# Performance work log

Hardware: AMD Instinct MI355X
Metric: run time of the kernel (lower is better)

The kernel has to match this reference:

```python
import jax, jax.numpy as jnp
import numpy as np

HEADS = 8
DIM_HEAD = 64
CHUNK = 128
EPS = 1e-6
KERNEL_EPS = 1e-4


def softmax_kernel(x, proj, is_query):
    # x: [b,h,n,d], proj: [f,d]  (FAVOR+ positive softmax features)
    d = x.shape[-1]
    data_normalizer = d ** -0.25
    ratio = proj.shape[0] ** -0.5
    data_dash = jnp.einsum('bhnd,fd->bhnf', x * data_normalizer, proj)
    diag = 0.5 * (data_normalizer ** 2) * jnp.sum(x * x, axis=-1, keepdims=True)  # [b,h,n,1]
    if is_query:
        m = jnp.max(data_dash, axis=-1, keepdims=True)
    else:
        m = jnp.max(data_dash, axis=(-1, -2), keepdims=True)
    return ratio * (jnp.exp(data_dash - diag - jax.lax.stop_gradient(m)) + KERNEL_EPS)


def infer_hidden_states(q, k, v, chunk_size=CHUNK):
    # q,k: [b,h,n,f], v: [b,h,n,e]; chunked causal linear attention with carried cumsums
    b, h, n, f = q.shape
    e = v.shape[-1]
    nc = n // chunk_size

    def to_chunks(t):
        return jnp.moveaxis(t.reshape(b, h, nc, chunk_size, t.shape[-1]), 2, 0)

    qs, ks, vs = to_chunks(q), to_chunks(k), to_chunks(v)

    def step(carry, inp):
        Z, S = carry  # [b,h,1,f], [b,h,1,f,e]
        qc, kc, vc = inp
        k_cum = Z + jnp.cumsum(kc, axis=2)                       # [b,h,c,f]
        D_inv = 1.0 / jnp.einsum('bhnf,bhnf->bhn', qc, k_cum + EPS)
        ctx = jnp.einsum('bhnf,bhne->bhnfe', kc, vc)             # [b,h,c,f,e]
        ctx_cum = S + jnp.cumsum(ctx, axis=2)
        out = jnp.einsum('bhnfe,bhnf,bhn->bhne', ctx_cum, qc, D_inv)
        return (k_cum[:, :, -1:], ctx_cum[:, :, -1:]), out

    init = (jnp.zeros((b, h, 1, f), q.dtype), jnp.zeros((b, h, 1, f, e), q.dtype))
    (Z, S), outs = jax.lax.scan(step, init, (qs, ks, vs))
    out = jnp.moveaxis(outs, 0, 2).reshape(b, h, n, e)
    return out, Z[:, :, 0], S[:, :, 0]


def reference(x, proj, Wq, Wk, Wv, Wo, bo):
    b, n, dim = x.shape
    h, dh = HEADS, DIM_HEAD

    def split_heads(t):
        return jnp.transpose(t.reshape(b, n, h, dh), (0, 2, 1, 3))

    q = split_heads(x @ Wq)
    k = split_heads(x @ Wk)
    v = split_heads(x @ Wv)

    qf = softmax_kernel(q, proj, is_query=True)
    kf = softmax_kernel(k, proj, is_query=False)

    out, Z, S = infer_hidden_states(qf, kf, v)
    out = jnp.transpose(out, (0, 2, 1, 3)).reshape(b, n, h * dh)
    out = out @ Wo + bo
    return out, Z, S


def setup_inputs() -> dict:
    key = jax.random.key(0)
    ks = jax.random.split(key, 6)
    b, n, dim = 2, 2048, 512
    f = 256
    return {
        'x': jax.random.normal(ks[0], (b, n, dim), jnp.float32),
        'proj': jax.random.normal(ks[1], (f, DIM_HEAD), jnp.float32),
        'Wq': jax.random.normal(ks[2], (dim, dim), jnp.float32) * (dim ** -0.5),
        'Wk': jax.random.normal(ks[3], (dim, dim), jnp.float32) * (dim ** -0.5),
        'Wv': jax.random.normal(ks[4], (dim, dim), jnp.float32) * (dim ** -0.5),
        'Wo': jax.random.normal(ks[5], (dim, dim), jnp.float32) * (dim ** -0.5),
        'bo': jnp.zeros((dim,), jnp.float32),
    }
```

## Files before the change

### kernel.cpp

```cpp
#include <hip/hip_runtime.h>
#include <hip/hip_bf16.h>
#include <math.h>

#define NB    2
#define NSEQ  2048
#define DIMM  512
#define NH    8
#define DHd   64
#define FF    256
#define CHK   128
#define NCHK  16
#define NBH   16

typedef unsigned short ushort_t;
typedef __attribute__((ext_vector_type(8))) __bf16 bf16x8;
typedef __attribute__((ext_vector_type(4))) float floatx4;

__device__ __forceinline__ unsigned short f2bf(float x) {
    union { __hip_bfloat16 h; unsigned short u; } v;
    v.h = __float2bfloat16(x);
    return v.u;
}
__device__ __forceinline__ float bf2f(unsigned short u) {
    union { unsigned short u2[2]; float f; } v;
    v.u2[0] = 0; v.u2[1] = u;
    return v.f;
}
__device__ __forceinline__ unsigned enc_f(float x) {
    unsigned u = __float_as_uint(x);
    return (u & 0x80000000u) ? ~u : (u | 0x80000000u);
}
__device__ __forceinline__ float dec_f(unsigned e) {
    unsigned u = (e & 0x80000000u) ? (e & 0x7fffffffu) : ~e;
    return __uint_as_float(u);
}

__device__ __forceinline__ void gload16(const void* g, void* l) {
    __builtin_amdgcn_global_load_lds(
        (const __attribute__((address_space(1))) void*)g,
        (__attribute__((address_space(3))) void*)l, 16, 0, 0);
}

__device__ __forceinline__ bf16x8 frag8(const ushort_t* lds, int row, int kb) {
    return *((const bf16x8*)lds + row * 8 + (kb ^ (row & 7)));
}
__device__ __forceinline__ bf16x8 fragS(const ushort_t* lds, int row, int kb) {
    return *((const bf16x8*)lds + row * 16 + (kb ^ (row & 15)));
}

__global__ __launch_bounds__(256)
void prep(const float* __restrict__ x, const float* __restrict__ proj,
          const float* __restrict__ W0, const float* __restrict__ W1,
          const float* __restrict__ W2, const float* __restrict__ W3,
          ushort_t* __restrict__ xb, ushort_t* __restrict__ projb,
          ushort_t* __restrict__ T0, ushort_t* __restrict__ T1,
          ushort_t* __restrict__ T2, ushort_t* __restrict__ T3,
          unsigned* __restrict__ mk_u)
{
    __shared__ float t[32][33];
    const int b = blockIdx.x, tid = threadIdx.x;
    if (b < 2048) {
        const int gid = b * 256 + tid;
        const float4 v = *(const float4*)(x + (size_t)gid * 4);
        union { ushort4 v4; unsigned short s[4]; } pk;
        pk.s[0] = f2bf(v.x); pk.s[1] = f2bf(v.y); pk.s[2] = f2bf(v.z); pk.s[3] = f2bf(v.w);
        ((ushort4*)xb)[gid] = pk.v4;
    } else if (b < 2064) {
        const int gid = (b - 2048) * 256 + tid;
        const float dn = 0.35355339059327379f;
        const float4 v = *(const float4*)(proj + (size_t)gid * 4);
        union { ushort4 v4; unsigned short s[4]; } pk;
        pk.s[0] = f2bf(v.x * dn); pk.s[1] = f2bf(v.y * dn);
        pk.s[2] = f2bf(v.z * dn); pk.s[3] = f2bf(v.w * dn);
        ((ushort4*)projb)[gid] = pk.v4;
    } else if (b < 3088) {
        const int idx = b - 2064;
        const int z = idx >> 8, rem = idx & 255;
        const int bx = rem & 15, by = rem >> 4;
        const float* W = (z == 0) ? W0 : (z == 1) ? W1 : (z == 2) ? W2 : W3;
        ushort_t* T = (z == 0) ? T0 : (z == 1) ? T1 : (z == 2) ? T2 : T3;
        const int x0 = bx * 32, y0 = by * 32;
        const int tx = tid & 31, ty = tid >> 5;
#pragma unroll
        for (int i = 0; i < 4; i++)
            t[ty + i * 8][tx] = W[(size_t)(y0 + ty + i * 8) * DIMM + x0 + tx];
        __syncthreads();
#pragma unroll
        for (int i = 0; i < 4; i++)
            T[(size_t)(x0 + ty + i * 8) * DIMM + y0 + tx] = f2bf(t[tx][ty + i * 8]);
    } else {
        if (tid < NBH) mk_u[tid] = 0u;
    }
}

__device__ __forceinline__ void mfma_mainloop(
    const ushort_t* __restrict__ AG, const ushort_t* __restrict__ BG,
    ushort_t* As, ushort_t* Bs, int ldA, int ldB, int K,
    floatx4 acc[4][4], int tid)
{
    const int lane = tid & 63, wid = tid >> 6;
    const int q = lane >> 4, c = lane & 15;
    const int wm = (wid >> 1) * 64, wn = (wid & 1) * 64;

    for (int k0 = 0; k0 < K; k0 += 64) {
#pragma unroll
        for (int t = 0; t < 4; t++) {
            const int g = t * 256 + tid, r = g >> 3, kb = (g & 7) ^ (r & 7);
            gload16(AG + (size_t)r * ldA + k0 + kb * 8, As + (size_t)g * 8);
        }
#pragma unroll
        for (int t = 0; t < 4; t++) {
            const int g = t * 256 + tid, r = g >> 3, kb = (g & 7) ^ (r & 7);
            gload16(BG + (size_t)r * ldB + k0 + kb * 8, Bs + (size_t)g * 8);
        }
        __syncthreads();
#pragma unroll
        for (int ks = 0; ks < 2; ks++) {
            bf16x8 af[4], bfr[4];
#pragma unroll
            for (int i = 0; i < 4; i++) {
                af[i]  = frag8(As, wm + i * 16 + c, ks * 4 + q);
                bfr[i] = frag8(Bs, wn + i * 16 + c, ks * 4 + q);
            }
#pragma unroll
            for (int i = 0; i < 4; i++)
#pragma unroll
                for (int j = 0; j < 4; j++)
                    acc[i][j] = __builtin_amdgcn_mfma_f32_16x16x32_bf16(
                        af[i], bfr[j], acc[i][j], 0, 0, 0);
        }
        __syncthreads();
    }
}

__global__ __launch_bounds__(256)
void gemm_qkv(const ushort_t* __restrict__ xb,
              const ushort_t* __restrict__ Wtq, const ushort_t* __restrict__ Wtk,
              const ushort_t* __restrict__ Wtv,
              ushort_t* __restrict__ qb, ushort_t* __restrict__ kb,
              ushort_t* __restrict__ vTb)
{
    __shared__ alignas(16) ushort_t SM[16896];
    ushort_t* As = SM;
    ushort_t* Bs = SM + 8192;
    const int tid = threadIdx.x;
    const int n0 = blockIdx.x * 128, m0 = blockIdx.y * 128, z = blockIdx.z;
    const ushort_t* Bt = (z == 0) ? Wtq : ((z == 1) ? Wtk : Wtv);

    floatx4 zero = {0.f, 0.f, 0.f, 0.f};
    floatx4 acc[4][4];
#pragma unroll
    for (int i = 0; i < 4; i++)
#pragma unroll
        for (int j = 0; j < 4; j++) acc[i][j] = zero;

    mfma_mainloop(xb + (size_t)m0 * DIMM, Bt + (size_t)n0 * DIMM, As, Bs,
                  DIMM, DIMM, DIMM, acc, tid);

    const int lane = tid & 63, wid = tid >> 6;
    const int q = lane >> 4, c = lane & 15;
    const int wm = (wid >> 1) * 64, wn = (wid & 1) * 64;

#pragma unroll
    for (int i = 0; i < 4; i++)
#pragma unroll
        for (int j = 0; j < 4; j++) {
            const int col = wn + j * 16 + c;
#pragma unroll
            for (int r = 0; r < 4; r++) {
                const int row = wm + i * 16 + q * 4 + r;
                SM[row * 132 + col] = f2bf(acc[i][j][r]);
            }
        }
    __syncthreads();

    if (z < 2) {
        ushort_t* ob = (z == 0) ? qb : kb;
#pragma unroll
        for (int p = 0; p < 16; p++) {
            const int idx = p * 256 + tid;
            const int row = idx >> 5, c4 = idx & 31;
            ushort4 o = *(const ushort4*)&SM[row * 132 + c4 * 4];
            *(ushort4*)(ob + (size_t)(m0 + row) * DIMM + n0 + c4 * 4) = o;
        }
    } else {
        const int bb = m0 >> 11, nbase = m0 & 2047;
#pragma unroll
        for (int p = 0; p < 16; p++) {
            const int idx = p * 256 + tid;
            const int cl2 = idx >> 5, n4 = idx & 31;
            const int C = n0 + cl2;
            const int h = C >> 6, e = C & 63;
            union { ushort4 v4; unsigned short s[4]; } pk;
#pragma unroll
            for (int k = 0; k < 4; k++) pk.s[k] = SM[(n4 * 4 + k) * 132 + cl2];
            *(ushort4*)(vTb + (((size_t)(bb * NH + h) * 64 + e)) * NSEQ + nbase + n4 * 4) = pk.v4;
        }
    }
}

__global__ __launch_bounds__(256)
void gemm_out(const ushort_t* __restrict__ attnb, const ushort_t* __restrict__ Wto,
              float* __restrict__ out, const float* __restrict__ bias)
{
    __shared__ alignas(16) ushort_t As[8192];
    __shared__ alignas(16) ushort_t Bs[8192];
    const int tid = threadIdx.x;
    const int n0 = blockIdx.x * 128, m0 = blockIdx.y * 128;

    floatx4 zero = {0.f, 0.f, 0.f, 0.f};
    floatx4 acc[4][4];
#pragma unroll
    for (int i = 0; i < 4; i++)
#pragma unroll
        for (int j = 0; j < 4; j++) acc[i][j] = zero;

    mfma_mainloop(attnb + (size_t)m0 * DIMM, Wto + (size_t)n0 * DIMM, As, Bs,
                  DIMM, DIMM, DIMM, acc, tid);

    const int lane = tid & 63, wid = tid >> 6;
    const int q = lane >> 4, c = lane & 15;
    const int wm = (wid >> 1) * 64, wn = (wid & 1) * 64;
#pragma unroll
    for (int i = 0; i < 4; i++)
#pragma unroll
        for (int j = 0; j < 4; j++) {
            const int col = n0 + wn + j * 16 + c;
            const float bv = bias[col];
#pragma unroll
            for (int r = 0; r < 4; r++) {
                const int row = m0 + wm + i * 16 + q * 4 + r;
                out[(size_t)row * DIMM + col] = acc[i][j][r] + bv;
            }
        }
}

__global__ __launch_bounds__(256)
void kmax(const ushort_t* __restrict__ kb_, const ushort_t* __restrict__ projb,
          unsigned* __restrict__ mk_u)
{
    __shared__ alignas(16) ushort_t As[8192];
    __shared__ alignas(16) ushort_t Bs[16384];
    __shared__ float red[256];
    const int tid = threadIdx.x, lane = tid & 63, wid = tid >> 6;
    const int q = lane >> 4, cl = lane & 15;
    const int m0 = blockIdx.x * 128, h = blockIdx.y;
    const int bb = m0 >> 11;
    const ushort_t* Aq = kb_ + (size_t)m0 * DIMM + h * 64;

#pragma unroll
    for (int t = 0; t < 4; t++) {
        const int g = t * 256 + tid, r = g >> 3, kb = (g & 7) ^ (r & 7);
        gload16(Aq + (size_t)r * DIMM + kb * 8, As + (size_t)g * 8);
    }
#pragma unroll
    for (int t = 0; t < 8; t++) {
        const int g = t * 256 + tid, r = g >> 3, kb = (g & 7) ^ (r & 7);
        gload16(projb + (size_t)r * 64 + kb * 8, Bs + (size_t)g * 8);
    }
    __syncthreads();

    floatx4 zero = {0.f, 0.f, 0.f, 0.f};
    floatx4 acc[4][8];
#pragma unroll
    for (int i = 0; i < 4; i++)
#pragma unroll
        for (int j = 0; j < 8; j++) acc[i][j] = zero;
    const int wm = (wid >> 1) * 64, wn = (wid & 1) * 128;
#pragma unroll
    for (int ks = 0; ks < 2; ks++) {
        bf16x8 af[4], bfr[8];
#pragma unroll
        for (int i = 0; i < 4; i++) af[i] = frag8(As, wm + i * 16 + cl, ks * 4 + q);
#pragma unroll
        for (int j = 0; j < 8; j++) bfr[j] = frag8(Bs, wn + j * 16 + cl, ks * 4 + q);
#pragma unroll
        for (int i = 0; i < 4; i++)
#pragma unroll
            for (int j = 0; j < 8; j++)
                acc[i][j] = __builtin_amdgcn_mfma_f32_16x16x32_bf16(
                    af[i], bfr[j], acc[i][j], 0, 0, 0);
    }
    float mloc = -3.0e38f;
#pragma unroll
    for (int i = 0; i < 4; i++)
#pragma unroll
        for (int j = 0; j < 8; j++)
#pragma unroll
            for (int r = 0; r < 4; r++) mloc = fmaxf(mloc, acc[i][j][r]);
    red[tid] = mloc;
    __syncthreads();
    for (int s = 128; s > 0; s >>= 1) {
        if (tid < s) red[tid] = fmaxf(red[tid], red[tid + s]);
        __syncthreads();
    }
    if (tid == 0) atomicMax(&mk_u[bb * NH + h], enc_f(red[0]));
}

__global__ __launch_bounds__(256)
void featx(const ushort_t* __restrict__ qb_, const ushort_t* __restrict__ kb_,
           const ushort_t* __restrict__ projb, const unsigned* __restrict__ mk_u,
           ushort_t* __restrict__ qfb, ushort_t* __restrict__ kfb,
           ushort_t* __restrict__ kfTb, float* __restrict__ Ksum)
{
    __shared__ alignas(16) ushort_t SM[24576];
    __shared__ float dtmp[256];
    __shared__ float diag_l[128];
    __shared__ float mx2[2][128];
    __shared__ float colp[2][256];
    ushort_t* As = SM;
    ushort_t* Bs = SM + 8192;
    const int tid = threadIdx.x, lane = tid & 63, wid = tid >> 6;
    const int q = lane >> 4, cl = lane & 15;
    const int m0 = blockIdx.x * 128, h = blockIdx.y, src = blockIdx.z;
    const int bb = m0 >> 11, nloc = m0 & 2047;
    const int bh = bb * NH + h;
    const int cidx = nloc >> 7;
    const ushort_t* Aq = (src ? kb_ : qb_) + (size_t)m0 * DIMM + h * 64;

    {
        const int row = tid >> 1, half = tid & 1;
        float s = 0.f;
        const ushort_t* p = Aq + (size_t)row * DIMM + half * 32;
#pragma unroll
        for (int d = 0; d < 32; d += 4) {
            ushort4 w = *(const ushort4*)(p + d);
            float a = bf2f(w.x), b2 = bf2f(w.y), c2 = bf2f(w.z), d2 = bf2f(w.w);
            s += a * a + b2 * b2 + c2 * c2 + d2 * d2;
        }
        dtmp[tid] = s;
    }
    __syncthreads();
    if (tid < 128) diag_l[tid] = (dtmp[2 * tid] + dtmp[2 * tid + 1]) * 0.0625f;

#pragma unroll
    for (int t = 0; t < 4; t++) {
        const int g = t * 256 + tid, r = g >> 3, kb = (g & 7) ^ (r & 7);
        gload16(Aq + (size_t)r * DIMM + kb * 8, As + (size_t)g * 8);
    }
#pragma unroll
    for (int t = 0; t < 8; t++) {
        const int g = t * 256 + tid, r = g >> 3, kb = (g & 7) ^ (r & 7);
        gload16(projb + (size_t)r * 64 + kb * 8, Bs + (size_t)g * 8);
    }
    __syncthreads();

    floatx4 zero = {0.f, 0.f, 0.f, 0.f};
    floatx4 acc[4][8];
#pragma unroll
    for (int i = 0; i < 4; i++)
#pragma unroll
        for (int j = 0; j < 8; j++) acc[i][j] = zero;
    const int wm = (wid >> 1) * 64, wn = (wid & 1) * 128;
#pragma unroll
    for (int ks = 0; ks < 2; ks++) {
        bf16x8 af[4], bfr[8];
#pragma unroll
        for (int i = 0; i < 4; i++) af[i] = frag8(As, wm + i * 16 + cl, ks * 4 + q);
#pragma unroll
        for (int j = 0; j < 8; j++) bfr[j] = frag8(Bs, wn + j * 16 + cl, ks * 4 + q);
#pragma unroll
        for (int i = 0; i < 4; i++)
#pragma unroll
            for (int j = 0; j < 8; j++)
                acc[i][j] = __builtin_amdgcn_mfma_f32_16x16x32_bf16(
                    af[i], bfr[j], acc[i][j], 0, 0, 0);
    }

    const float mk = src ? dec_f(mk_u[bh]) : 0.f;
    if (src == 0) {
#pragma unroll
        for (int i = 0; i < 4; i++)
#pragma unroll
            for (int r = 0; r < 4; r++) {
                const int row = wm + i * 16 + q * 4 + r;
                float mx = -3.0e38f;
#pragma unroll
                for (int j = 0; j < 8; j++) mx = fmaxf(mx, acc[i][j][r]);
                mx = fmaxf(mx, __shfl_xor(mx, 1)); mx = fmaxf(mx, __shfl_xor(mx, 2));
                mx = fmaxf(mx, __shfl_xor(mx, 4)); mx = fmaxf(mx, __shfl_xor(mx, 8));
                if (cl == 0) mx2[wid & 1][row] = mx;
            }
    }
    __syncthreads();

#pragma unroll
    for (int i = 0; i < 4; i++)
#pragma unroll
        for (int r = 0; r < 4; r++) {
            const int row = wm + i * 16 + q * 4 + r;
            const float cc = diag_l[row] + (src ? mk : fmaxf(mx2[0][row], mx2[1][row]));
#pragma unroll
            for (int j = 0; j < 8; j++)
                acc[i][j][r] = 0.0625f * (__expf(acc[i][j][r] - cc) + 1.0e-4f);
        }

    if (src) {
#pragma unroll
        for (int j = 0; j < 8; j++) {
            float s = 0.f;
#pragma unroll
            for (int i = 0; i < 4; i++)
                s += acc[i][j][0] + acc[i][j][1] + acc[i][j][2] + acc[i][j][3];
            s += __shfl_xor(s, 16);
            s += __shfl_xor(s, 32);
            if (q == 0) colp[wid >> 1][wn + j * 16 + cl] = s;
        }
    }

    ushort_t* ff = src ? kfb : qfb;
    const size_t frow = (size_t)bh * NSEQ + nloc;

#pragma unroll
    for (int hf = 0; hf < 2; hf++) {
        __syncthreads();
        if ((wid & 1) == hf) {
#pragma unroll
            for (int i = 0; i < 4; i++)
#pragma unroll
                for (int j = 0; j < 8; j++) {
                    const int col = j * 16 + cl;
#pragma unroll
                    for (int r = 0; r < 4; r++) {
                        const int row = wm + i * 16 + q * 4 + r;
                        SM[row * 132 + col] = f2bf(acc[i][j][r]);
                    }
                }
        }
        if (hf == 0 && src) {
            Ksum[((size_t)bh * NCHK + cidx) * FF + tid] = colp[0][tid] + colp[1][tid];
        }
        __syncthreads();
#pragma unroll
        for (int p = 0; p < 16; p++) {
            const int idx = p * 256 + tid;
            const int row = idx >> 5, c4 = idx & 31;
            ushort4 o = *(const ushort4*)&SM[row * 132 + c4 * 4];
            *(ushort4*)(ff + (frow + row) * FF + hf * 128 + c4 * 4) = o;
        }
        if (src) {
#pragma unroll
            for (int p = 0; p < 16; p++) {
                const int idx = p * 256 + tid;
                const int f = idx >> 5, n4 = idx & 31;
                union { ushort4 v4; unsigned short s[4]; } pk;
#pragma unroll
                for (int k = 0; k < 4; k++) pk.s[k] = SM[(n4 * 4 + k) * 132 + f];
                *(ushort4*)(kfTb + ((size_t)bh * FF + hf * 128 + f) * NSEQ + nloc + n4 * 4) = pk.v4;
            }
        }
    }
}

__global__ __launch_bounds__(256)
void ctx_mfma(const ushort_t* __restrict__ vTb, const ushort_t* __restrict__ kfTb,
              float* __restrict__ CTXT)
{
    __shared__ alignas(16) ushort_t As[4096];
    __shared__ alignas(16) ushort_t Bs[16384];
    const int tid = threadIdx.x, lane = tid & 63, wid = tid >> 6;
    const int q = lane >> 4, cl = lane & 15;
    const int bh = blockIdx.x >> 4, c = blockIdx.x & 15;
    const ushort_t* A = vTb + ((size_t)bh * 64) * NSEQ + c * CHK;
    const ushort_t* B = kfTb + ((size_t)bh * FF) * NSEQ + c * CHK;
    const int fw = wid * 64;

    floatx4 zero = {0.f, 0.f, 0.f, 0.f};
    floatx4 acc[4][4];
#pragma unroll
    for (int i = 0; i < 4; i++)
#pragma unroll
        for (int j = 0; j < 4; j++) acc[i][j] = zero;

    for (int k0 = 0; k0 < CHK; k0 += 64) {
#pragma unroll
        for (int t = 0; t < 2; t++) {
            const int g = t * 256 + tid, r = g >> 3, kb = (g & 7) ^ (r & 7);
            gload16(A + (size_t)r * NSEQ + k0 + kb * 8, As + (size_t)g * 8);
        }
#pragma unroll
        for (int t = 0; t < 8; t++) {
            const int g = t * 256 + tid, r = g >> 3, kb = (g & 7) ^ (r & 7);
            gload16(B + (size_t)r * NSEQ + k0 + kb * 8, Bs + (size_t)g * 8);
        }
        __syncthreads();
#pragma unroll
        for (int ks = 0; ks < 2; ks++) {
            bf16x8 af[4], bfr[4];
#pragma unroll
            for (int i = 0; i < 4; i++) {
                af[i]  = frag8(As, i * 16 + cl, ks * 4 + q);
                bfr[i] = frag8(Bs, fw + i * 16 + cl, ks * 4 + q);
            }
#pragma unroll
            for (int i = 0; i < 4; i++)
#pragma unroll
                for (int j = 0; j < 4; j++)
                    acc[i][j] = __builtin_amdgcn_mfma_f32_16x16x32_bf16(
                        af[i], bfr[j], acc[i][j], 0, 0, 0);
        }
        __syncthreads();
    }
#pragma unroll
    for (int i = 0; i < 4; i++)
#pragma unroll
        for (int j = 0; j < 4; j++) {
            const int f = fw + j * 16 + cl;
#pragma unroll
            for (int r = 0; r < 4; r++) {
                const int e = i * 16 + q * 4 + r;
                CTXT[(((size_t)bh * NCHK + c) * 64 + e) * FF + f] = acc[i][j][r];
            }
        }
}

__global__ void prefix_zs(float* __restrict__ Ksum, float* __restrict__ Zout,
                          const float* __restrict__ CTXT, ushort_t* __restrict__ ctxp,
                          float* __restrict__ Sout)
{
    const int b = blockIdx.x;
    if (b < 1024) {
        const int idx = b * 256 + threadIdx.x;
        const int bh = idx >> 14, ef = idx & 16383;
        const int e = ef >> 8, f = ef & 255;
        float run = 0.f;
#pragma unroll
        for (int c = 0; c < NCHK; c++) {
            const size_t o = (((size_t)bh * NCHK + c) * 64 + e) * FF + f;
            const float t = CTXT[o];
            ctxp[o] = f2bf(run);
            run += t;
        }
        Sout[((size_t)bh * FF + f) * 64 + e] = run;
    } else {
        const int idx = (b - 1024) * 256 + threadIdx.x;
        const int bh = idx >> 8, f = idx & 255;
        float run = 0.f;
#pragma unroll
        for (int c = 0; c < NCHK; c++) {
            const size_t o = ((size_t)(bh * NCHK + c)) * FF + f;
            const float t = Ksum[o];
            Ksum[o] = run;
            run += t;
        }
        Zout[(size_t)bh * FF + f] = run;
    }
}

__global__ __launch_bounds__(256)
void chunk_out_mfma(const ushort_t* __restrict__ qfb, const ushort_t* __restrict__ kfb,
                    const ushort_t* __restrict__ vTb, const float* __restrict__ Zex,
                    const ushort_t* __restrict__ ctxp, ushort_t* __restrict__ attnb)
{
    __shared__ alignas(16) ushort_t Sld[16384];
    __shared__ alignas(16) ushort_t As[8192];
    __shared__ alignas(16) ushort_t Bs[8192];
    __shared__ float zeps[256];
    __shared__ float rows_part[2][128];
    __shared__ float denp[256];
    __shared__ float den_l[128];

    const int tid = threadIdx.x, lane = tid & 63, wid = tid >> 6;
    const int q = lane >> 4, cl = lane & 15;
    const int bh = blockIdx.x >> 4, c = blockIdx.x & 15;
    const int bb = bh >> 3, h = bh & 7;
    const int n0 = c * CHK;
    const ushort_t* Q  = qfb + ((size_t)bh * NSEQ + n0) * FF;
    const ushort_t* Kf = kfb + ((size_t)bh * NSEQ + n0) * FF;

    zeps[tid] = Zex[((size_t)bh * NCHK + c) * FF + tid] + 1.0e-6f;

    floatx4 zero = {0.f, 0.f, 0.f, 0.f};
    floatx4 acc1[4][4];
#pragma unroll
    for (int i = 0; i < 4; i++)
#pragma unroll
        for (int j = 0; j < 4; j++) acc1[i][j] = zero;
    const int wm = (wid >> 1) * 64, wn = (wid & 1) * 64;
    for (int k0 = 0; k0 < FF; k0 += 64) {
#pragma unroll
        for (int t = 0; t < 4; t++) {
            const int g = t * 256 + tid, r = g >> 3, kb = (g & 7) ^ (r & 7);
            gload16(Q + (size_t)r * FF + k0 + kb * 8, As + (size_t)g * 8);
        }
#pragma unroll
        for (int t = 0; t < 4; t++) {
            const int g = t * 256 + tid, r = g >> 3, kb = (g & 7) ^ (r & 7);
            gload16(Kf + (size_t)r * FF + k0 + kb * 8, Bs + (size_t)g * 8);
        }
        __syncthreads();
#pragma unroll
        for (int ks = 0; ks < 2; ks++) {
            bf16x8 af[4], bfr[4];
#pragma unroll
            for (int i = 0; i < 4; i++) {
                af[i]  = frag8(As, wm + i * 16 + cl, ks * 4 + q);
                bfr[i] = frag8(Bs, wn + i * 16 + cl, ks * 4 + q);
            }
#pragma unroll
            for (int i = 0; i < 4; i++)
#pragma unroll
                for (int j = 0; j < 4; j++)
                    acc1[i][j] = __builtin_amdgcn_mfma_f32_16x16x32_bf16(
                        af[i], bfr[j], acc1[i][j], 0, 0, 0);
        }
        __syncthreads();
    }
#pragma unroll
    for (int i = 0; i < 4; i++)
#pragma unroll
        for (int r = 0; r < 4; r++) {
            const int row = wm + i * 16 + q * 4 + r;
            float part = 0.f;
#pragma unroll
            for (int j = 0; j < 4; j++) {
                const int col = wn + j * 16 + cl;
                const float v = (col <= row) ? acc1[i][j][r] : 0.f;
                part += v;
                Sld[(row * 16 + ((col >> 3) ^ (row & 15))) * 8 + (col & 7)] = f2bf(v);
            }
            part += __shfl_xor(part, 1); part += __shfl_xor(part, 2);
            part += __shfl_xor(part, 4); part += __shfl_xor(part, 8);
            if (cl == 0) rows_part[wid & 1][row] = part;
        }
    __syncthreads();

    floatx4 acc2[4][2];
#pragma unroll
    for (int i = 0; i < 4; i++)
#pragma unroll
        for (int j = 0; j < 2; j++) acc2[i][j] = zero;
    const ushort_t* Vt = vTb + ((size_t)bh * 64) * NSEQ + n0;
    for (int k0 = 0; k0 < CHK; k0 += 64) {
#pragma unroll
        for (int t = 0; t < 2; t++) {
            const int g = t * 256 + tid, r = g >> 3, kb = (g & 7) ^ (r & 7);
            gload16(Vt + (size_t)r * NSEQ + k0 + kb * 8, As + (size_t)g * 8);
        }
        __syncthreads();
#pragma unroll
        for (int ks = 0; ks < 2; ks++) {
            bf16x8 af[4], bfr[2];
            const int kbS = (k0 >> 3) + ks * 4 + q;
#pragma unroll
            for (int i = 0; i < 4; i++) af[i] = frag8(As, i * 16 + cl, ks * 4 + q);
#pragma unroll
            for (int j = 0; j < 2; j++) bfr[j] = fragS(Sld, wid * 32 + j * 16 + cl, kbS);
#pragma unroll
            for (int i = 0; i < 4; i++)
#pragma unroll
                for (int j = 0; j < 2; j++)
                    acc2[i][j] = __builtin_amdgcn_mfma_f32_16x16x32_bf16(
                        af[i], bfr[j], acc2[i][j], 0, 0, 0);
        }
        __syncthreads();
    }

    const ushort_t* Cp = ctxp + ((size_t)bh * NCHK + c) * 64 * FF;
    float dacc = 0.f;
    const int drow = tid & 127, dhalf = tid >> 7;
    for (int k0 = 0; k0 < FF; k0 += 64) {
#pragma unroll
        for (int t = 0; t < 2; t++) {
            const int g = t * 256 + tid, r = g >> 3, kb = (g & 7) ^ (r & 7);
            gload16(Cp + (size_t)r * FF + k0 + kb * 8, As + (size_t)g * 8);
        }
#pragma unroll
        for (int t = 0; t < 4; t++) {
            const int g = t * 256 + tid, r = g >> 3, kb = (g & 7) ^ (r & 7);
            gload16(Q + (size_t)r * FF + k0 + kb * 8, Bs + (size_t)g * 8);
        }
        __syncthreads();
#pragma unroll
        for (int ks = 0; ks < 2; ks++) {
            bf16x8 af[4], bfr[2];
#pragma unroll
            for (int i = 0; i < 4; i++) af[i] = frag8(As, i * 16 + cl, ks * 4 + q);
#pragma unroll
            for (int j = 0; j < 2; j++) bfr[j] = frag8(Bs, wid * 32 + j * 16 + cl, ks * 4 + q);
#pragma unroll
            for (int i = 0; i < 4; i++)
#pragma unroll
                for (int j = 0; j < 2; j++)
                    acc2[i][j] = __builtin_amdgcn_mfma_f32_16x16x32_bf16(
                        af[i], bfr[j], acc2[i][j], 0, 0, 0);
        }
#pragma unroll
        for (int gi = 0; gi < 4; gi++) {
            const int kb = dhalf * 4 + gi;
            const ushort_t* gp = Bs + ((size_t)drow * 8 + (kb ^ (drow & 7))) * 8;
            const int kbase = k0 + kb * 8;
#pragma unroll
            for (int e2 = 0; e2 < 8; e2++)
                dacc = fmaf(bf2f(gp[e2]), zeps[kbase + e2], dacc);
        }
        __syncthreads();
    }
    denp[tid] = dacc;
    __syncthreads();
    if (tid < 128)
        den_l[tid] = rows_part[0][tid] + rows_part[1][tid] + denp[tid] + denp[tid + 128];
    __syncthreads();

#pragma unroll
    for (int j = 0; j < 2; j++) {
        const int row = wid * 32 + j * 16 + cl;
        const float dinv = 1.0f / den_l[row];
#pragma unroll
        for (int i = 0; i < 4; i++)
#pragma unroll
            for (int r = 0; r < 4; r++) {
                const int e = i * 16 + q * 4 + r;
                Sld[row * 68 + e] = f2bf(acc2[i][j][r] * dinv);
            }
    }
    __syncthreads();
#pragma unroll
    for (int p = 0; p < 8; p++) {
        const int idx = p * 256 + tid;
        const int row = idx >> 4, e4 = idx & 15;
        ushort4 o = *(const ushort4*)&Sld[row * 68 + e4 * 4];
        *(ushort4*)(attnb + ((size_t)(bb * NSEQ + n0 + row)) * DIMM + h * 64 + e4 * 4) = o;
    }
}

extern "C" void kernel_launch(void* const* d_in, const int* in_sizes, int n_in,
                              void* d_out, int out_size, void* d_ws, size_t ws_size,
                              hipStream_t stream)
{
    (void)in_sizes; (void)n_in; (void)out_size; (void)ws_size;
    const float* x    = (const float*)d_in[0];
    const float* proj = (const float*)d_in[1];
    const float* Wq   = (const float*)d_in[2];
    const float* Wk   = (const float*)d_in[3];
    const float* Wv   = (const float*)d_in[4];
    const float* Wo   = (const float*)d_in[5];
    const float* bo   = (const float*)d_in[6];
    float* out = (float*)d_out;

    char* W = (char*)d_ws;
    float*    CTXT = (float*)W;              W += (size_t)16777216;
    ushort_t* kfTb = (ushort_t*)W;           W += (size_t)16777216;
    ushort_t* qfb  = (ushort_t*)W;           W += (size_t)16777216;
    ushort_t* kfb  = (ushort_t*)W;           W += (size_t)16777216;
    ushort_t* qb   = (ushort_t*)W;           W += (size_t)4194304;
    ushort_t* kb   = (ushort_t*)W;           W += (size_t)4194304;
    ushort_t* xb   = (ushort_t*)W;           W += (size_t)4194304;
    ushort_t* vTb  = (ushort_t*)W;           W += (size_t)4194304;
    ushort_t* Wtq  = (ushort_t*)W;           W += (size_t)524288;
    ushort_t* Wtk  = (ushort_t*)W;           W += (size_t)524288;
    ushort_t* Wtv  = (ushort_t*)W;           W += (size_t)524288;
    ushort_t* Wto  = (ushort_t*)W;           W += (size_t)524288;
    ushort_t* projb = (ushort_t*)W;          W += (size_t)32768;
    float*    Ksum = (float*)W;              W += (size_t)262144;
    unsigned* mk_u = (unsigned*)W;           W += (size_t)256;

    ushort_t* ctxp = qb;
    ushort_t* attnb = xb;

    float* Zout = out + (size_t)4096 * 512;
    float* Sout = Zout + (size_t)NBH * FF;

    hipLaunchKernelGGL(prep, dim3(3089), dim3(256), 0, stream,
                       x, proj, Wq, Wk, Wv, Wo, xb, projb, Wtq, Wtk, Wtv, Wto, mk_u);
    hipLaunchKernelGGL(gemm_qkv, dim3(4, 32, 3), dim3(256), 0, stream,
                       xb, Wtq, Wtk, Wtv, qb, kb, vTb);
    hipLaunchKernelGGL(kmax, dim3(32, 8), dim3(256), 0, stream, kb, projb, mk_u);
    hipLaunchKernelGGL(featx, dim3(32, 8, 2), dim3(256), 0, stream,
                       qb, kb, projb, mk_u, qfb, kfb, kfTb, Ksum);
    hipLaunchKernelGGL(ctx_mfma, dim3(256), dim3(256), 0, stream, vTb, kfTb, CTXT);
    hipLaunchKernelGGL(prefix_zs, dim3(1040), dim3(256), 0, stream,
                       Ksum, Zout, CTXT, ctxp, Sout);
    hipLaunchKernelGGL(chunk_out_mfma, dim3(256), dim3(256), 0, stream,
                       qfb, kfb, vTb, Ksum, ctxp, attnb);
    hipLaunchKernelGGL(gemm_out, dim3(4, 32), dim3(256), 0, stream, attnb, Wto, out, bo);
}
```

Measured before the change: 165.7 us.

## Fuse per-chunk context GEMM into feature kernel, drop transposed key features

The key-feature path of featx now computes the per-chunk V^T·kf context product directly from its register accumulators, staging feature tiles in shared memory, and writes CTXT. This removes the separate ctx_mfma launch and the 16 MB transposed kfTb buffer write and re-read. In exchange, the key blocks of featx do extra MFMA work with added barriers, so query and key blocks become imbalanced. The bf16 rounding of features is unchanged.

```diff
diff --git a/kernel.cpp b/kernel.cpp
--- a/kernel.cpp
+++ b/kernel.cpp
@@ -300,8 +300,9 @@
 __global__ __launch_bounds__(256)
 void featx(const ushort_t* __restrict__ qb_, const ushort_t* __restrict__ kb_,
            const ushort_t* __restrict__ projb, const unsigned* __restrict__ mk_u,
+           const ushort_t* __restrict__ vTb,
            ushort_t* __restrict__ qfb, ushort_t* __restrict__ kfb,
-           ushort_t* __restrict__ kfTb, float* __restrict__ Ksum)
+           float* __restrict__ CTXT, float* __restrict__ Ksum)
 {
     __shared__ alignas(16) ushort_t SM[24576];
     __shared__ float dtmp[256];
@@ -438,80 +439,60 @@
             ushort4 o = *(const ushort4*)&SM[row * 132 + c4 * 4];
             *(ushort4*)(ff + (frow + row) * FF + hf * 128 + c4 * 4) = o;
         }
-        if (src) {
-#pragma unroll
-            for (int p = 0; p < 16; p++) {
-                const int idx = p * 256 + tid;
-                const int f = idx >> 5, n4 = idx & 31;
-                union { ushort4 v4; unsigned short s[4]; } pk;
-#pragma unroll
-                for (int k = 0; k < 4; k++) pk.s[k] = SM[(n4 * 4 + k) * 132 + f];
-                *(ushort4*)(kfTb + ((size_t)bh * FF + hf * 128 + f) * NSEQ + nloc + n4 * 4) = pk.v4;
-            }
-        }
-    }
-}
-
-__global__ __launch_bounds__(256)
-void ctx_mfma(const ushort_t* __restrict__ vTb, const ushort_t* __restrict__ kfTb,
-              float* __restrict__ CTXT)
-{
-    __shared__ alignas(16) ushort_t As[4096];
-    __shared__ alignas(16) ushort_t Bs[16384];
-    const int tid = threadIdx.x, lane = tid & 63, wid = tid >> 6;
-    const int q = lane >> 4, cl = lane & 15;
-    const int bh = blockIdx.x >> 4, c = blockIdx.x & 15;
-    const ushort_t* A = vTb + ((size_t)bh * 64) * NSEQ + c * CHK;
-    const ushort_t* B = kfTb + ((size_t)bh * FF) * NSEQ + c * CHK;
-    const int fw = wid * 64;
-
-    floatx4 zero = {0.f, 0.f, 0.f, 0.f};
-    floatx4 acc[4][4];
-#pragma unroll
-    for (int i = 0; i < 4; i++)
-#pragma unroll
-        for (int j = 0; j < 4; j++) acc[i][j] = zero;
-
-    for (int k0 = 0; k0 < CHK; k0 += 64) {
-#pragma unroll
-        for (int t = 0; t < 2; t++) {
-            const int g = t * 256 + tid, r = g >> 3, kb = (g & 7) ^ (r & 7);
-            gload16(A + (size_t)r * NSEQ + k0 + kb * 8, As + (size_t)g * 8);
-        }
-#pragma unroll
-        for (int t = 0; t < 8; t++) {
-            const int g = t * 256 + tid, r = g >> 3, kb = (g & 7) ^ (r & 7);
-            gload16(B + (size_t)r * NSEQ + k0 + kb * 8, Bs + (size_t)g * 8);
-        }
-        __syncthreads();
-#pragma unroll
-        for (int ks = 0; ks < 2; ks++) {
-            bf16x8 af[4], bfr[4];
-#pragma unroll
-            for (int i = 0; i < 4; i++) {
-                af[i]  = frag8(As, i * 16 + cl, ks * 4 + q);
-                bfr[i] = frag8(Bs, fw + i * 16 + cl, ks * 4 + q);
-            }
-#pragma unroll
-            for (int i = 0; i < 4; i++)
-#pragma unroll
-                for (int j = 0; j < 4; j++)
-                    acc[i][j] = __builtin_amdgcn_mfma_f32_16x16x32_bf16(
-                        af[i], bfr[j], acc[i][j], 0, 0, 0);
-        }
-        __syncthreads();
-    }
-#pragma unroll
-    for (int i = 0; i < 4; i++)
-#pragma unroll
-        for (int j = 0; j < 4; j++) {
-            const int f = fw + j * 16 + cl;
+    }
+
+    if (src == 0) return;
+
+    __syncthreads();
+    ushort_t* Vs = SM;
+    ushort_t* T  = SM + 8192;
+    const ushort_t* Vg = vTb + ((size_t)bh * 64) * NSEQ + nloc;
+#pragma unroll
+    for (int t = 0; t < 4; t++) {
+        const int g = t * 256 + tid, r = g >> 4, kb = (g & 15) ^ (r & 15);
+        gload16(Vg + (size_t)r * NSEQ + kb * 8, Vs + (size_t)g * 8);
+    }
+
+    const size_t cbase = ((size_t)bh * NCHK + cidx) * 64;
+#pragma unroll
+    for (int fq = 0; fq < 4; fq++) {
+        if ((wid & 1) == (fq >> 1)) {
+#pragma unroll
+            for (int jj = 0; jj < 4; jj++) {
+                const int j = (fq & 1) * 4 + jj;
+#pragma unroll
+                for (int i = 0; i < 4; i++)
+#pragma unroll
+                    for (int r = 0; r < 4; r++) {
+                        const int n = wm + i * 16 + q * 4 + r;
+                        T[(jj * 16 + cl) * 136 + n] = f2bf(acc[i][j][r]);
+                    }
+            }
+        }
+        __syncthreads();
+        floatx4 accc[4];
+#pragma unroll
+        for (int jj = 0; jj < 4; jj++) accc[jj] = zero;
+#pragma unroll
+        for (int kt = 0; kt < 4; kt++) {
+            const bf16x8 av = fragS(Vs, wid * 16 + cl, kt * 4 + q);
+#pragma unroll
+            for (int jj = 0; jj < 4; jj++) {
+                const bf16x8 bv = *(const bf16x8*)(T + (jj * 16 + cl) * 136 + (kt * 4 + q) * 8);
+                accc[jj] = __builtin_amdgcn_mfma_f32_16x16x32_bf16(av, bv, accc[jj], 0, 0, 0);
+            }
+        }
+#pragma unroll
+        for (int jj = 0; jj < 4; jj++) {
+            const int f = fq * 64 + jj * 16 + cl;
 #pragma unroll
             for (int r = 0; r < 4; r++) {
-                const int e = i * 16 + q * 4 + r;
-                CTXT[(((size_t)bh * NCHK + c) * 64 + e) * FF + f] = acc[i][j][r];
-            }
-        }
+                const int e = wid * 16 + q * 4 + r;
+                CTXT[(cbase + e) * FF + f] = accc[jj][r];
+            }
+        }
+        __syncthreads();
+    }
 }
 
 __global__ void prefix_zs(float* __restrict__ Ksum, float* __restrict__ Zout,
@@ -740,7 +721,6 @@
 
     char* W = (char*)d_ws;
     float*    CTXT = (float*)W;              W += (size_t)16777216;
-    ushort_t* kfTb = (ushort_t*)W;           W += (size_t)16777216;
     ushort_t* qfb  = (ushort_t*)W;           W += (size_t)16777216;
     ushort_t* kfb  = (ushort_t*)W;           W += (size_t)16777216;
     ushort_t* qb   = (ushort_t*)W;           W += (size_t)4194304;
@@ -767,8 +747,7 @@
                        xb, Wtq, Wtk, Wtv, qb, kb, vTb);
     hipLaunchKernelGGL(kmax, dim3(32, 8), dim3(256), 0, stream, kb, projb, mk_u);
     hipLaunchKernelGGL(featx, dim3(32, 8, 2), dim3(256), 0, stream,
-                       qb, kb, projb, mk_u, qfb, kfb, kfTb, Ksum);
-    hipLaunchKernelGGL(ctx_mfma, dim3(256), dim3(256), 0, stream, vTb, kfTb, CTXT);
+                       qb, kb, projb, mk_u, vTb, qfb, kfb, CTXT, Ksum);
     hipLaunchKernelGGL(prefix_zs, dim3(1040), dim3(256), 0, stream,
                        Ksum, Zout, CTXT, ctxp, Sout);
     hipLaunchKernelGGL(chunk_out_mfma, dim3(256), dim3(256), 0, stream,
```

Result: faster. 157.3 us (-5.1%).
